# Kernel optimization log

Measured on AMD Instinct MI355X. Metric: run time of the kernel, lower is better.

## Reference

```python
import jax, jax.numpy as jnp
import numpy as np

NUM_CHANNELS = 256
NUM_HEADS = 8
HEAD_DIM = NUM_CHANNELS // NUM_HEADS


def setup_inputs() -> dict:
    key = jax.random.key(0)
    k1, k2, k3, k4, k5 = jax.random.split(key, 5)
    C = NUM_CHANNELS
    s = 1.0 / np.sqrt(C)
    image = jax.random.normal(k1, (8, C, 32, 32), dtype=jnp.float32)
    # kqv_projection: Linear(C, 3C); mix_heads: Linear(C, C). Stored as [in, out].
    w_kqv = jax.random.uniform(k2, (C, 3 * C), minval=-s, maxval=s, dtype=jnp.float32)
    b_kqv = jax.random.uniform(k3, (3 * C,), minval=-s, maxval=s, dtype=jnp.float32)
    w_mix = jax.random.uniform(k4, (C, C), minval=-s, maxval=s, dtype=jnp.float32)
    b_mix = jax.random.uniform(k5, (C,), minval=-s, maxval=s, dtype=jnp.float32)
    return {"image": image, "w_kqv": w_kqv, "b_kqv": b_kqv, "w_mix": w_mix, "b_mix": b_mix}


def _masked_attention(seq, w_kqv, b_kqv, w_mix, b_mix):
    # seq: [N, T, C]
    N, T, C = seq.shape
    H, D = NUM_HEADS, HEAD_DIM
    projected = seq @ w_kqv + b_kqv            # [N, T, 3C]
    k, q, v = jnp.split(projected, 3, axis=-1)  # order: keys, queries, values
    # split heads -> [N, H, T, D]
    k = k.reshape(N, T, H, D).transpose(0, 2, 1, 3)
    q = q.reshape(N, T, H, D).transpose(0, 2, 1, 3)
    v = v.reshape(N, T, H, D).transpose(0, 2, 1, 3)
    logits = jnp.einsum('nhtd,nhsd->nhts', q, k) / jnp.sqrt(jnp.float32(D))
    causal = jnp.tril(jnp.ones((T, T), dtype=bool))
    logits = jnp.where(causal, logits, -jnp.inf)
    weights = jax.nn.softmax(logits, axis=-1)
    out = jnp.einsum('nhts,nhsd->nhtd', weights, v)  # [N, H, T, D]
    out = out.transpose(0, 2, 1, 3).reshape(N, T, C)  # combine heads
    return out @ w_mix + b_mix


def reference(image, w_kqv, b_kqv, w_mix, b_mix):
    N, C, Hh, Ww = image.shape
    seq = image.transpose(0, 2, 3, 1).reshape(N, Hh * Ww, C)
    attn = _masked_attention(seq, w_kqv, b_kqv, w_mix, b_mix)
    attn = attn.reshape(N, Hh, Ww, C).transpose(0, 3, 1, 2)
    return attn + image
```

## Files before the change

kernel.cpp:

```cpp
#include <hip/hip_runtime.h>
#include <math.h>

constexpr int NB  = 8;
constexpr int C   = 256;
constexpr int T   = 1024;
constexpr int NH  = 8;
constexpr int HD  = 32;
constexpr int C3  = 768;

constexpr float QSCALE = 0.25503489422229562f;

typedef __attribute__((ext_vector_type(8))) short bf16x8;
typedef __attribute__((ext_vector_type(4))) float f32x4;

__device__ inline short f2bf(float f) {
    unsigned u = __float_as_uint(f);
    u += 0x7FFF + ((u >> 16) & 1);
    return (short)(u >> 16);
}
__device__ inline short f2bf_trunc(float f) {
    return (short)(__float_as_uint(f) >> 16);
}

__device__ __forceinline__ void gl16(const void* g, void* l) {
    __builtin_amdgcn_global_load_lds(
        (const __attribute__((address_space(1))) unsigned int*)g,
        (__attribute__((address_space(3))) unsigned int*)l, 16, 0, 0);
}

__global__ __launch_bounds__(256) void prep_tc(const float* __restrict__ image,
                                               const float* __restrict__ wkqv,
                                               const float* __restrict__ wmix,
                                               short* __restrict__ Xb,
                                               short* __restrict__ Wkb,
                                               short* __restrict__ Wmb) {
    __shared__ float tile[64][65];
    const int bid = blockIdx.x;
    const int tid = threadIdx.x;
    const float* src; short* dst;
    int Cc, r0, c0;
    if (bid < 512) {
        const int nb = bid >> 6, t = bid & 63;
        src = image + (size_t)nb * C * T;
        dst = Xb + (size_t)nb * T * C;
        Cc = T; r0 = (t & 3) * 64; c0 = (t >> 2) * 64;
    } else if (bid < 560) {
        const int t = bid - 512;
        src = wkqv; dst = Wkb;
        Cc = C3; r0 = (t & 3) * 64; c0 = (t >> 2) * 64;
    } else {
        const int t = bid - 560;
        src = wmix; dst = Wmb;
        Cc = C; r0 = (t & 3) * 64; c0 = (t >> 2) * 64;
    }
    const int lr = tid >> 4, lc = (tid & 15) * 4;
    #pragma unroll
    for (int p = 0; p < 4; ++p) {
        float4 v = *(const float4*)&src[(size_t)(r0 + 16 * p + lr) * Cc + c0 + lc];
        tile[16 * p + lr][lc + 0] = v.x;
        tile[16 * p + lr][lc + 1] = v.y;
        tile[16 * p + lr][lc + 2] = v.z;
        tile[16 * p + lr][lc + 3] = v.w;
    }
    __syncthreads();
    const int wc = tid >> 2, wr = (tid & 3) * 16;
    bf16x8 v0, v1;
    #pragma unroll
    for (int e = 0; e < 8; ++e) v0[e] = f2bf(tile[wr + e][wc]);
    #pragma unroll
    for (int e = 0; e < 8; ++e) v1[e] = f2bf(tile[wr + 8 + e][wc]);
    short* o = dst + (size_t)(c0 + wc) * C + r0 + wr;
    *(bf16x8*)&o[0] = v0;
    *(bf16x8*)&o[8] = v1;
}

__global__ __launch_bounds__(256) void kqv_mfma(const short* __restrict__ Xb,
                                                const short* __restrict__ Wkb,
                                                const float* __restrict__ bkqv,
                                                short* __restrict__ Kb,
                                                short* __restrict__ Qb,
                                                short* __restrict__ Vtb) {
    __shared__ __align__(16) short As[128 * 64];
    __shared__ __align__(16) short Bs[64 * 64];
    const int tid = threadIdx.x;
    const int n0 = blockIdx.x * 64;
    const int m0 = blockIdx.y * 128;
    const int nb = m0 >> 10, t0 = m0 & 1023;
    const int wv = tid >> 6, lane = tid & 63;
    const int m = lane & 15, quad = lane >> 4;

    const short* Xn = Xb + (size_t)nb * T * C + (size_t)t0 * C;
    const short* Wn = Wkb + (size_t)n0 * C;

    f32x4 acc[2][4];
    const f32x4 z = {0.f, 0.f, 0.f, 0.f};
    #pragma unroll
    for (int i = 0; i < 2; ++i)
        #pragma unroll
        for (int j = 0; j < 4; ++j) acc[i][j] = z;

    const int sx = (m & 7) << 4;

    for (int k0 = 0; k0 < C; k0 += 64) {
        #pragma unroll
        for (int p = 0; p < 4; ++p) {
            const int o = p * 4096 + tid * 16;
            const int row = o >> 7;
            const int cb = (o & 127) ^ ((row & 7) << 4);
            gl16(Xn + (size_t)row * C + k0 + (cb >> 1), (char*)As + o);
        }
        #pragma unroll
        for (int p = 0; p < 2; ++p) {
            const int o = p * 4096 + tid * 16;
            const int row = o >> 7;
            const int cb = (o & 127) ^ ((row & 7) << 4);
            gl16(Wn + (size_t)row * C + k0 + (cb >> 1), (char*)Bs + o);
        }
        __syncthreads();

        bf16x8 a[2][2], b[2][4];
        #pragma unroll
        for (int kk = 0; kk < 2; ++kk) {
            #pragma unroll
            for (int i = 0; i < 2; ++i)
                a[kk][i] = *(const bf16x8*)((const char*)As +
                            (32 * wv + 16 * i + m) * 128 + ((kk * 64 + quad * 16) ^ sx));
            #pragma unroll
            for (int j = 0; j < 4; ++j)
                b[kk][j] = *(const bf16x8*)((const char*)Bs +
                            (16 * j + m) * 128 + ((kk * 64 + quad * 16) ^ sx));
        }
        #pragma unroll
        for (int kk = 0; kk < 2; ++kk)
            #pragma unroll
            for (int i = 0; i < 2; ++i)
                #pragma unroll
                for (int j = 0; j < 4; ++j)
                    acc[i][j] = __builtin_amdgcn_mfma_f32_16x16x32_bf16(a[kk][i], b[kk][j], acc[i][j], 0, 0, 0);
        __syncthreads();
    }

    #pragma unroll
    for (int j = 0; j < 4; ++j) {
        int jj = n0 + 16 * j + m;
        int chunk = jj >> 8, hh = (jj >> 5) & 7, d = jj & 31;
        float bias = bkqv[jj];
        if (chunk < 2) {
            short* dst = (chunk == 0) ? Kb : Qb;
            float mul = (chunk == 1) ? QSCALE : 1.0f;
            size_t base = (size_t)(nb * NH + hh) * T * HD + d;
            #pragma unroll
            for (int i = 0; i < 2; ++i) {
                int t = t0 + 32 * wv + 16 * i + 4 * quad;
                #pragma unroll
                for (int r = 0; r < 4; ++r)
                    dst[base + (size_t)(t + r) * HD] = f2bf((acc[i][j][r] + bias) * mul);
            }
        } else {
            size_t base = (size_t)(nb * NH + hh) * (16 * 2048) + (size_t)d * 64;
            #pragma unroll
            for (int i = 0; i < 2; ++i) {
                #pragma unroll
                for (int r = 0; r < 4; ++r) {
                    int t = t0 + 32 * wv + 16 * i + 4 * quad + r;
                    Vtb[base + (size_t)(t >> 6) * 2048 + (t & 63)] = f2bf(acc[i][j][r] + bias);
                }
            }
        }
    }
}

__global__ __launch_bounds__(256) void attn_mfma(const short* __restrict__ Kb,
                                                 const short* __restrict__ Qb,
                                                 const short* __restrict__ Vtb,
                                                 short* __restrict__ attnb) {
    const int qb = (blockIdx.z & 4) ? 7 - blockIdx.x : blockIdx.x;
    const int h  = blockIdx.y;
    const int nb = blockIdx.z;
    const int tid  = threadIdx.x;
    const int wv   = tid >> 6;
    const int lane = tid & 63;
    const int m    = lane & 15;
    const int quad = lane >> 4;

    __shared__ __align__(16) short Ps[128][72];

    const int q0  = qb * 128;
    const int nstw = 2 * qb + 1 + (wv >> 1);
    const size_t hb = (size_t)(nb * NH + h) * T * HD;
    const short* Kp = Kb + hb;
    const short* Qp = Qb + hb;
    const short* Vp = Vtb + (size_t)(nb * NH + h) * (16 * 2048);
    const f32x4 z = {0.f, 0.f, 0.f, 0.f};

    bf16x8 aq[2];
    #pragma unroll
    for (int i = 0; i < 2; ++i)
        aq[i] = *(const bf16x8*)&Qp[(size_t)(q0 + 32 * wv + 16 * i + m) * HD + 8 * quad];

    bf16x8 bk[4], vb[2][2];
    #pragma unroll
    for (int j = 0; j < 4; ++j)
        bk[j] = *(const bf16x8*)&Kp[(size_t)(16 * j + m) * HD + 8 * quad];
    #pragma unroll
    for (int kc = 0; kc < 2; ++kc)
        #pragma unroll
        for (int hf = 0; hf < 2; ++hf)
            vb[kc][hf] = *(const bf16x8*)&Vp[(size_t)(16 * hf + m) * 64 + 32 * kc + 8 * quad];

    f32x4 O[2][2] = {{z, z}, {z, z}};
    float lp[2][2] = {{0.f, 0.f}, {0.f, 0.f}};

    auto step = [&](const int st, const bool msk) {
        f32x4 S[2][4];
        #pragma unroll
        for (int i = 0; i < 2; ++i)
            #pragma unroll
            for (int j = 0; j < 4; ++j)
                S[i][j] = __builtin_amdgcn_mfma_f32_16x16x32_bf16(bk[j], aq[i], z, 0, 0, 0);

        if (st + 1 < nstw) {
            #pragma unroll
            for (int j = 0; j < 4; ++j)
                bk[j] = *(const bf16x8*)&Kp[(size_t)((st + 1) * 64 + 16 * j + m) * HD + 8 * quad];
        }

        const int s0 = st * 64;
        #pragma unroll
        for (int i = 0; i < 2; ++i) {
            const int qr = q0 + 32 * wv + 16 * i + m;
            #pragma unroll
            for (int j = 0; j < 4; ++j) {
                const int kb = s0 + 16 * j + 4 * quad;
                float e0 = __builtin_amdgcn_exp2f(S[i][j][0]);
                float e1 = __builtin_amdgcn_exp2f(S[i][j][1]);
                float e2 = __builtin_amdgcn_exp2f(S[i][j][2]);
                float e3 = __builtin_amdgcn_exp2f(S[i][j][3]);
                if (msk) {
                    if (kb + 0 > qr) e0 = 0.f;
                    if (kb + 1 > qr) e1 = 0.f;
                    if (kb + 2 > qr) e2 = 0.f;
                    if (kb + 3 > qr) e3 = 0.f;
                }
                lp[i][j & 1] += (e0 + e1) + (e2 + e3);
                short4 p4 = { f2bf_trunc(e0), f2bf_trunc(e1),
                              f2bf_trunc(e2), f2bf_trunc(e3) };
                *(short4*)&Ps[32 * wv + 16 * i + m][16 * j + 4 * quad] = p4;
            }
        }

        #pragma unroll
        for (int kc = 0; kc < 2; ++kc) {
            bf16x8 ap0 = *(const bf16x8*)&Ps[32 * wv + m][32 * kc + 8 * quad];
            bf16x8 ap1 = *(const bf16x8*)&Ps[32 * wv + 16 + m][32 * kc + 8 * quad];
            O[0][0] = __builtin_amdgcn_mfma_f32_16x16x32_bf16(ap0, vb[kc][0], O[0][0], 0, 0, 0);
            O[0][1] = __builtin_amdgcn_mfma_f32_16x16x32_bf16(ap0, vb[kc][1], O[0][1], 0, 0, 0);
            O[1][0] = __builtin_amdgcn_mfma_f32_16x16x32_bf16(ap1, vb[kc][0], O[1][0], 0, 0, 0);
            O[1][1] = __builtin_amdgcn_mfma_f32_16x16x32_bf16(ap1, vb[kc][1], O[1][1], 0, 0, 0);
        }

        if (st + 1 < nstw) {
            const short* Vn = Vp + (size_t)(st + 1) * 2048;
            #pragma unroll
            for (int kc = 0; kc < 2; ++kc)
                #pragma unroll
                for (int hf = 0; hf < 2; ++hf)
                    vb[kc][hf] = *(const bf16x8*)&Vn[(size_t)(16 * hf + m) * 64 + 32 * kc + 8 * quad];
        }
    };

    const int mq = 2 * qb;
    for (int st = 0; st < mq; ++st) step(st, false);
    for (int st = mq; st < nstw; ++st) step(st, true);

    #pragma unroll
    for (int i = 0; i < 2; ++i) {
        float l = lp[i][0] + lp[i][1];
        l += __shfl_xor(l, 16);
        l += __shfl_xor(l, 32);
        #pragma unroll
        for (int r = 0; r < 4; ++r) {
            float lr = __shfl(l, 4 * quad + r);
            float inv = 1.f / lr;
            int row = q0 + 32 * wv + 16 * i + 4 * quad + r;
            short* op = attnb + ((size_t)(nb * T + row)) * C + h * HD;
            op[m]      = f2bf(O[i][0][r] * inv);
            op[16 + m] = f2bf(O[i][1][r] * inv);
        }
    }
}

__global__ __launch_bounds__(256) void mix_mfma(const short* __restrict__ attnb,
                                                const short* __restrict__ Wmb,
                                                const float* __restrict__ bmix,
                                                const float* __restrict__ image,
                                                float* __restrict__ out) {
    __shared__ __align__(16) short Bs[64][264];
    const int tid = threadIdx.x;
    const int n0 = blockIdx.x * 64;
    const int m0 = blockIdx.y * 64;
    const int nb = m0 >> 10, t0 = m0 & 1023;
    const int wv = tid >> 6, lane = tid & 63;
    const int m = lane & 15, quad = lane >> 4;

    {
        const short* wrow = Wmb + (size_t)(n0 + (tid >> 2)) * C + (tid & 3) * 64;
        short* brow = &Bs[tid >> 2][(tid & 3) * 64];
        #pragma unroll
        for (int g = 0; g < 8; ++g)
            *(bf16x8*)&brow[8 * g] = *(const bf16x8*)&wrow[8 * g];
    }
    __syncthreads();

    f32x4 acc[4];
    const f32x4 z = {0.f, 0.f, 0.f, 0.f};
    #pragma unroll
    for (int j = 0; j < 4; ++j) acc[j] = z;

    #pragma unroll
    for (int k0 = 0; k0 < C; k0 += 32) {
        bf16x8 a = *(const bf16x8*)&attnb[(size_t)(m0 + 16 * wv + m) * C + k0 + 8 * quad];
        bf16x8 b[4];
        #pragma unroll
        for (int j = 0; j < 4; ++j) b[j] = *(const bf16x8*)&Bs[16 * j + m][k0 + 8 * quad];
        #pragma unroll
        for (int j = 0; j < 4; ++j)
            acc[j] = __builtin_amdgcn_mfma_f32_16x16x32_bf16(a, b[j], acc[j], 0, 0, 0);
    }

    const int tb = t0 + 16 * wv + 4 * quad;
    #pragma unroll
    for (int j = 0; j < 4; ++j) {
        int c = n0 + 16 * j + m;
        float bias = bmix[c];
        size_t o = (size_t)(nb * C + c) * T + tb;
        float4 img = *(const float4*)&image[o];
        float4 res = { acc[j][0] + bias + img.x,
                       acc[j][1] + bias + img.y,
                       acc[j][2] + bias + img.z,
                       acc[j][3] + bias + img.w };
        *(float4*)&out[o] = res;
    }
}

extern "C" void kernel_launch(void* const* d_in, const int* in_sizes, int n_in,
                              void* d_out, int out_size, void* d_ws, size_t ws_size,
                              hipStream_t stream) {
    const float* image = (const float*)d_in[0];
    const float* w_kqv = (const float*)d_in[1];
    const float* b_kqv = (const float*)d_in[2];
    const float* w_mix = (const float*)d_in[3];
    const float* b_mix = (const float*)d_in[4];
    float* out = (float*)d_out;

    short* Xb    = (short*)d_ws;
    short* Wkb   = Xb  + (size_t)NB * T * C;
    short* Wmb   = Wkb + (size_t)C3 * C;
    short* Kb    = Wmb + (size_t)C * C;
    short* Qb    = Kb  + (size_t)NB * NH * T * HD;
    short* Vtb   = Qb  + (size_t)NB * NH * T * HD;
    short* attnb = Vtb + (size_t)NB * NH * T * HD;

    prep_tc<<<576, 256, 0, stream>>>(image, w_kqv, w_mix, Xb, Wkb, Wmb);
    kqv_mfma<<<dim3(C3 / 64, NB * T / 128), 256, 0, stream>>>(Xb, Wkb, b_kqv, Kb, Qb, Vtb);
    attn_mfma<<<dim3(8, NH, NB), 256, 0, stream>>>(Kb, Qb, Vtb, attnb);
    mix_mfma<<<dim3(C / 64, NB * T / 64), 256, 0, stream>>>(attnb, Wmb, b_mix, image, out);
}
```

Before: 102.2 us.

## Software-pipeline QK^T MFMAs in attention and remap GEMM blocks per XCD

The attention kernel now double-buffers the K fragments and score tiles, issuing the QK^T MFMAs for the next key step before the exp/mask/PV work of the current one, and prefetching K two steps ahead. The aim is to hide MFMA and global-load latency behind the softmax math. The projection and mix GEMMs switch to a 1D grid with an index remap that places the column tiles sharing a row tile on the same XCD, which should improve L2 reuse of the activation rows. The cost is more live registers in attention, which could lower occupancy.

After: 109.0 us. +6.7%, slower.

```diff
diff --git a/kernel.cpp b/kernel.cpp
--- a/kernel.cpp
+++ b/kernel.cpp
@@ -20,6 +20,10 @@
 }
 __device__ inline short f2bf_trunc(float f) {
     return (short)(__float_as_uint(f) >> 16);
+}
+
+__device__ __forceinline__ f32x4 mfma32(bf16x8 a, bf16x8 b, f32x4 c) {
+    return __builtin_amdgcn_mfma_f32_16x16x32_bf16(a, b, c, 0, 0, 0);
 }
 
 __device__ __forceinline__ void gl16(const void* g, void* l) {
@@ -83,8 +87,13 @@
     __shared__ __align__(16) short As[128 * 64];
     __shared__ __align__(16) short Bs[64 * 64];
     const int tid = threadIdx.x;
-    const int n0 = blockIdx.x * 64;
-    const int m0 = blockIdx.y * 128;
+    const int bid = blockIdx.x;
+    const int xcd = bid & 7;
+    const int kq  = bid >> 3;
+    const int nt  = kq % 12;
+    const int mt  = (kq / 12) * 8 + xcd;
+    const int n0 = nt * 64;
+    const int m0 = mt * 128;
     const int nb = m0 >> 10, t0 = m0 & 1023;
     const int wv = tid >> 6, lane = tid & 63;
     const int m = lane & 15, quad = lane >> 4;
@@ -136,7 +145,7 @@
             for (int i = 0; i < 2; ++i)
                 #pragma unroll
                 for (int j = 0; j < 4; ++j)
-                    acc[i][j] = __builtin_amdgcn_mfma_f32_16x16x32_bf16(a[kk][i], b[kk][j], acc[i][j], 0, 0, 0);
+                    acc[i][j] = mfma32(a[kk][i], b[kk][j], acc[i][j]);
         __syncthreads();
     }
 
@@ -186,7 +195,8 @@
     __shared__ __align__(16) short Ps[128][72];
 
     const int q0  = qb * 128;
-    const int nstw = 2 * qb + 1 + (wv >> 1);
+    const int mq  = 2 * qb;
+    const int nstw = mq + 1 + (wv >> 1);
     const size_t hb = (size_t)(nb * NH + h) * T * HD;
     const short* Kp = Kb + hb;
     const short* Qp = Qb + hb;
@@ -198,10 +208,10 @@
     for (int i = 0; i < 2; ++i)
         aq[i] = *(const bf16x8*)&Qp[(size_t)(q0 + 32 * wv + 16 * i + m) * HD + 8 * quad];
 
-    bf16x8 bk[4], vb[2][2];
+    bf16x8 bkA[4], bkB[4], vb[2][2];
     #pragma unroll
     for (int j = 0; j < 4; ++j)
-        bk[j] = *(const bf16x8*)&Kp[(size_t)(16 * j + m) * HD + 8 * quad];
+        bkA[j] = *(const bf16x8*)&Kp[(size_t)(16 * j + m) * HD + 8 * quad];
     #pragma unroll
     for (int kc = 0; kc < 2; ++kc)
         #pragma unroll
@@ -211,18 +221,33 @@
     f32x4 O[2][2] = {{z, z}, {z, z}};
     float lp[2][2] = {{0.f, 0.f}, {0.f, 0.f}};
 
-    auto step = [&](const int st, const bool msk) {
-        f32x4 S[2][4];
-        #pragma unroll
-        for (int i = 0; i < 2; ++i)
-            #pragma unroll
-            for (int j = 0; j < 4; ++j)
-                S[i][j] = __builtin_amdgcn_mfma_f32_16x16x32_bf16(bk[j], aq[i], z, 0, 0, 0);
-
-        if (st + 1 < nstw) {
-            #pragma unroll
-            for (int j = 0; j < 4; ++j)
-                bk[j] = *(const bf16x8*)&Kp[(size_t)((st + 1) * 64 + 16 * j + m) * HD + 8 * quad];
+    f32x4 SA[2][4], SB[2][4];
+    #pragma unroll
+    for (int i = 0; i < 2; ++i)
+        #pragma unroll
+        for (int j = 0; j < 4; ++j)
+            SA[i][j] = mfma32(bkA[j], aq[i], z);
+    if (nstw > 1) {
+        #pragma unroll
+        for (int j = 0; j < 4; ++j)
+            bkB[j] = *(const bf16x8*)&Kp[(size_t)(64 + 16 * j + m) * HD + 8 * quad];
+    }
+
+    auto step = [&](f32x4 (&Sc)[2][4], f32x4 (&Sn)[2][4],
+                    bf16x8 (&bkN)[4], bf16x8 (&bkL)[4],
+                    const int st, const bool msk) {
+        const bool hasNext = (st + 1 < nstw);
+        if (hasNext) {
+            #pragma unroll
+            for (int i = 0; i < 2; ++i)
+                #pragma unroll
+                for (int j = 0; j < 4; ++j)
+                    Sn[i][j] = mfma32(bkN[j], aq[i], z);
+            if (st + 2 < nstw) {
+                #pragma unroll
+                for (int j = 0; j < 4; ++j)
+                    bkL[j] = *(const bf16x8*)&Kp[(size_t)((st + 2) * 64 + 16 * j + m) * HD + 8 * quad];
+            }
         }
 
         const int s0 = st * 64;
@@ -232,10 +257,10 @@
             #pragma unroll
             for (int j = 0; j < 4; ++j) {
                 const int kb = s0 + 16 * j + 4 * quad;
-                float e0 = __builtin_amdgcn_exp2f(S[i][j][0]);
-                float e1 = __builtin_amdgcn_exp2f(S[i][j][1]);
-                float e2 = __builtin_amdgcn_exp2f(S[i][j][2]);
-                float e3 = __builtin_amdgcn_exp2f(S[i][j][3]);
+                float e0 = __builtin_amdgcn_exp2f(Sc[i][j][0]);
+                float e1 = __builtin_amdgcn_exp2f(Sc[i][j][1]);
+                float e2 = __builtin_amdgcn_exp2f(Sc[i][j][2]);
+                float e3 = __builtin_amdgcn_exp2f(Sc[i][j][3]);
                 if (msk) {
                     if (kb + 0 > qr) e0 = 0.f;
                     if (kb + 1 > qr) e1 = 0.f;
@@ -253,13 +278,13 @@
         for (int kc = 0; kc < 2; ++kc) {
             bf16x8 ap0 = *(const bf16x8*)&Ps[32 * wv + m][32 * kc + 8 * quad];
             bf16x8 ap1 = *(const bf16x8*)&Ps[32 * wv + 16 + m][32 * kc + 8 * quad];
-            O[0][0] = __builtin_amdgcn_mfma_f32_16x16x32_bf16(ap0, vb[kc][0], O[0][0], 0, 0, 0);
-            O[0][1] = __builtin_amdgcn_mfma_f32_16x16x32_bf16(ap0, vb[kc][1], O[0][1], 0, 0, 0);
-            O[1][0] = __builtin_amdgcn_mfma_f32_16x16x32_bf16(ap1, vb[kc][0], O[1][0], 0, 0, 0);
-            O[1][1] = __builtin_amdgcn_mfma_f32_16x16x32_bf16(ap1, vb[kc][1], O[1][1], 0, 0, 0);
-        }
-
-        if (st + 1 < nstw) {
+            O[0][0] = mfma32(ap0, vb[kc][0], O[0][0]);
+            O[0][1] = mfma32(ap0, vb[kc][1], O[0][1]);
+            O[1][0] = mfma32(ap1, vb[kc][0], O[1][0]);
+            O[1][1] = mfma32(ap1, vb[kc][1], O[1][1]);
+        }
+
+        if (hasNext) {
             const short* Vn = Vp + (size_t)(st + 1) * 2048;
             #pragma unroll
             for (int kc = 0; kc < 2; ++kc)
@@ -269,9 +294,15 @@
         }
     };
 
-    const int mq = 2 * qb;
-    for (int st = 0; st < mq; ++st) step(st, false);
-    for (int st = mq; st < nstw; ++st) step(st, true);
+    int st = 0;
+    for (; st < mq; ++st) {
+        if (st & 1) step(SB, SA, bkA, bkB, st, false);
+        else        step(SA, SB, bkB, bkA, st, false);
+    }
+    for (; st < nstw; ++st) {
+        if (st & 1) step(SB, SA, bkA, bkB, st, true);
+        else        step(SA, SB, bkB, bkA, st, true);
+    }
 
     #pragma unroll
     for (int i = 0; i < 2; ++i) {
@@ -297,8 +328,13 @@
                                                 float* __restrict__ out) {
     __shared__ __align__(16) short Bs[64][264];
     const int tid = threadIdx.x;
-    const int n0 = blockIdx.x * 64;
-    const int m0 = blockIdx.y * 64;
+    const int bid = blockIdx.x;
+    const int xcd = bid & 7;
+    const int kq  = bid >> 3;
+    const int nt  = kq & 3;
+    const int mt  = (kq >> 2) * 8 + xcd;
+    const int n0 = nt * 64;
+    const int m0 = mt * 64;
     const int nb = m0 >> 10, t0 = m0 & 1023;
     const int wv = tid >> 6, lane = tid & 63;
     const int m = lane & 15, quad = lane >> 4;
@@ -325,7 +361,7 @@
         for (int j = 0; j < 4; ++j) b[j] = *(const bf16x8*)&Bs[16 * j + m][k0 + 8 * quad];
         #pragma unroll
         for (int j = 0; j < 4; ++j)
-            acc[j] = __builtin_amdgcn_mfma_f32_16x16x32_bf16(a, b[j], acc[j], 0, 0, 0);
+            acc[j] = mfma32(a, b[j], acc[j]);
     }
 
     const int tb = t0 + 16 * wv + 4 * quad;
@@ -362,7 +398,7 @@
     short* attnb = Vtb + (size_t)NB * NH * T * HD;
 
     prep_tc<<<576, 256, 0, stream>>>(image, w_kqv, w_mix, Xb, Wkb, Wmb);
-    kqv_mfma<<<dim3(C3 / 64, NB * T / 128), 256, 0, stream>>>(Xb, Wkb, b_kqv, Kb, Qb, Vtb);
+    kqv_mfma<<<dim3(768), 256, 0, stream>>>(Xb, Wkb, b_kqv, Kb, Qb, Vtb);
     attn_mfma<<<dim3(8, NH, NB), 256, 0, stream>>>(Kb, Qb, Vtb, attnb);
-    mix_mfma<<<dim3(C / 64, NB * T / 64), 256, 0, stream>>>(attnb, Wmb, b_mix, image, out);
-}
+    mix_mfma<<<dim3(512), 256, 0, stream>>>(attnb, Wmb, b_mix, image, out);
+}
```
